# Optimization experiments

Hardware: AMD Instinct MI355X
Metric: run time of the kernel (lower is better)

## Reference

```python
import jax, jax.numpy as jnp
import numpy as np

NUM_HEADS = 16

def setup_inputs() -> dict:
    key = jax.random.key(0)
    ks = jax.random.split(key, 5)
    b, n, d = 2, 2048, 1024
    s = 0.02
    return {
        "x": jax.random.normal(ks[0], (b, n, d), jnp.float32),
        "wq": jax.random.normal(ks[1], (d, d), jnp.float32) * s,
        "wk": jax.random.normal(ks[2], (d, d), jnp.float32) * s,
        "wv": jax.random.normal(ks[3], (d, d), jnp.float32) * s,
        "wo": jax.random.normal(ks[4], (d, d), jnp.float32) * s,
        "bo": jnp.zeros((d,), jnp.float32),
    }

def reference(x, wq, wk, wv, wo, bo):
    b, n, c = x.shape
    h = NUM_HEADS
    hd = c // h
    scale = hd ** -0.5
    # qkv projections (qkv_bias=False); torch Linear computes x @ W.T
    def split_heads(t):
        return t.reshape(b, n, h, hd).transpose(0, 2, 1, 3)  # b h n d
    q = split_heads(x @ wq.T)
    k = split_heads(x @ wk.T)
    v = split_heads(x @ wv.T)
    dots = jnp.einsum('bhid,bhjd->bhij', q, k) * scale
    attn = jax.nn.softmax(dots, axis=-1)  # attn_drop=0 -> identity
    out = jnp.einsum('bhij,bhjd->bhid', attn, v)
    out = out.transpose(0, 2, 1, 3).reshape(b, n, c)
    out = out @ wo.T + bo  # proj_drop=0 -> identity
    return out
```

## Files before the change

kernel.cpp:

```cpp
#include <hip/hip_runtime.h>
#include <hip/hip_bf16.h>

typedef float f32x4 __attribute__((ext_vector_type(4)));
typedef short short8 __attribute__((ext_vector_type(8)));
typedef short short4v __attribute__((ext_vector_type(4)));

#define MFMA(a, b, c) __builtin_amdgcn_mfma_f32_16x16x32_bf16((a), (b), (c), 0, 0, 0)

#if __has_builtin(__builtin_amdgcn_exp2f)
#define EXP2(x) __builtin_amdgcn_exp2f(x)
#else
#define EXP2(x) exp2f(x)
#endif

#define B_  2
#define N_  2048
#define C_  1024
#define H_  16
#define HD_ 64
#define M_  (B_ * N_)

#define QSCALE 0.18033688011112042f

typedef const __attribute__((address_space(1))) void* gp_t;
typedef __attribute__((address_space(3))) void* sp_t;
#define GLL16(g, s) __builtin_amdgcn_global_load_lds((gp_t)(const void*)(g), (sp_t)(void*)(s), 16, 0, 0)

__device__ __forceinline__ short f2bf(float f) {
    union { float fv; unsigned u; } v; v.fv = f;
    unsigned r = v.u + 0x7fffu + ((v.u >> 16) & 1u);
    return (short)(r >> 16);
}
__device__ __forceinline__ unsigned pack_rne(float a, float b) {
    return (unsigned)(unsigned short)f2bf(a) | ((unsigned)(unsigned short)f2bf(b) << 16);
}

__global__ __launch_bounds__(256) void convert_kernel(
    const float* __restrict__ x,  const float* __restrict__ wq,
    const float* __restrict__ wk, const float* __restrict__ wv,
    const float* __restrict__ wo, short* __restrict__ dst)
{
    size_t e = ((size_t)blockIdx.x * 256 + threadIdx.x) * 8;
    const float* src; size_t off;
    if (e < 4194304)      { src = x;  off = e; }
    else if (e < 5242880) { src = wq; off = e - 4194304; }
    else if (e < 6291456) { src = wk; off = e - 5242880; }
    else if (e < 7340032) { src = wv; off = e - 6291456; }
    else                  { src = wo; off = e - 7340032; }
    float4 a = *(const float4*)(src + off);
    float4 b = *(const float4*)(src + off + 4);
    short8 s;
    s[0] = f2bf(a.x); s[1] = f2bf(a.y); s[2] = f2bf(a.z); s[3] = f2bf(a.w);
    s[4] = f2bf(b.x); s[5] = f2bf(b.y); s[6] = f2bf(b.z); s[7] = f2bf(b.w);
    *(short8*)(dst + e) = s;
}

__global__ __launch_bounds__(256) void qkv_gemm(
    const short* __restrict__ xb, const short* __restrict__ Wb,
    short* __restrict__ Qb, short* __restrict__ Kb, short* __restrict__ Vt)
{
    const int m0 = blockIdx.x * 128;
    const int n0 = blockIdx.y * 128;
    __shared__ short As[128 * 64];
    __shared__ short Bs[128 * 64];
    const int tid  = threadIdx.x;
    const int wave = tid >> 6, lane = tid & 63;
    const int quad = lane >> 4, l16 = lane & 15;
    const int wr = (wave >> 1) * 64, wc = (wave & 1) * 64;
    const int sw = l16 & 7;

    const int rS = tid >> 3;
    const int cS = (tid & 7) ^ (rS & 7);
    const short* A_src = xb + (size_t)(m0 + rS) * C_ + cS * 8;
    const short* B_src = Wb + (size_t)(n0 + rS) * C_ + cS * 8;

    f32x4 acc[4][4] = {};

    for (int kk = 0; kk < C_; kk += 64) {
        __syncthreads();
        #pragma unroll
        for (int it = 0; it < 4; ++it) {
            GLL16(A_src + (size_t)(it * 32) * C_ + kk, &As[it * 2048 + tid * 8]);
            GLL16(B_src + (size_t)(it * 32) * C_ + kk, &Bs[it * 2048 + tid * 8]);
        }
        __syncthreads();
        short8 af[4][2], bf[4][2];
        #pragma unroll
        for (int mi = 0; mi < 4; ++mi) {
            int row = (wr + mi * 16 + l16) * 64;
            af[mi][0] = *(const short8*)&As[row + ((quad    ) ^ sw) * 8];
            af[mi][1] = *(const short8*)&As[row + ((quad + 4) ^ sw) * 8];
        }
        #pragma unroll
        for (int ni = 0; ni < 4; ++ni) {
            int row = (wc + ni * 16 + l16) * 64;
            bf[ni][0] = *(const short8*)&Bs[row + ((quad    ) ^ sw) * 8];
            bf[ni][1] = *(const short8*)&Bs[row + ((quad + 4) ^ sw) * 8];
        }
        #pragma unroll
        for (int k2 = 0; k2 < 2; ++k2)
        #pragma unroll
        for (int mi = 0; mi < 4; ++mi)
        #pragma unroll
        for (int ni = 0; ni < 4; ++ni)
            acc[mi][ni] = MFMA(af[mi][k2], bf[ni][k2], acc[mi][ni]);
    }

    const int which = n0 >> 10;
    const int nb = n0 & 1023;
    #pragma unroll
    for (int mi = 0; mi < 4; ++mi)
    #pragma unroll
    for (int ni = 0; ni < 4; ++ni)
    #pragma unroll
    for (int r = 0; r < 4; ++r) {
        int m  = m0 + wr + mi * 16 + quad * 4 + r;
        int cc = nb + wc + ni * 16 + l16;
        float av = acc[mi][ni][r];
        if (which == 0) av *= QSCALE;
        short bv = f2bf(av);
        int bb = m >> 11, ns = m & (N_ - 1);
        int h = cc >> 6, d = cc & 63;
        size_t bh = (size_t)(bb * H_ + h);
        if (which == 0)      Qb[(bh * N_ + ns) * HD_ + d] = bv;
        else if (which == 1) Kb[(bh * N_ + ns) * HD_ + d] = bv;
        else                 Vt[(bh * HD_ + d) * N_ + ns] = bv;
    }
}

__global__ __launch_bounds__(256, 4) void attn_split(
    const short* __restrict__ Qb, const short* __restrict__ Kb,
    const short* __restrict__ Vt, float* __restrict__ Opart,
    float* __restrict__ lpart)
{
    const int bid = blockIdx.x;
    const int swz = (bid & 7) * 128 + (bid >> 3);
    const int bh = swz >> 5;
    const int i0 = ((swz >> 1) & 15) * 128;
    const int sp = swz & 1;
    __shared__ short Ks[2][64 * 64];
    __shared__ short Vs[2][64 * 64];
    const int tid  = threadIdx.x;
    const int wave = tid >> 6, lane = tid & 63;
    const int quad = lane >> 4, l16 = lane & 15;
    const int sw = l16 & 7;

    const short* Qg = Qb + ((size_t)bh * N_ + i0) * HD_;
    const short* Kg = Kb + (size_t)bh * N_ * HD_;
    const short* Vg = Vt + (size_t)bh * HD_ * N_;

    const int row0 = tid >> 3,  c0 = (tid & 7) ^ (row0 & 7);
    const int row1 = row0 + 32, c1 = (tid & 7) ^ (row1 & 7);
    const short* KgA0 = Kg + (sp * 1024 + row0) * HD_ + c0 * 8;
    const short* KgA1 = Kg + (sp * 1024 + row1) * HD_ + c1 * 8;
    const short* VgA0 = Vg + (size_t)row0 * N_ + sp * 1024 + c0 * 8;
    const short* VgA1 = Vg + (size_t)row1 * N_ + sp * 1024 + c1 * 8;

    short8 qf[2][2];
    #pragma unroll
    for (int s = 0; s < 2; ++s) {
        const short* qrow = Qg + (wave * 32 + s * 16 + l16) * HD_;
        qf[s][0] = *(const short8*)(qrow + quad * 8);
        qf[s][1] = *(const short8*)(qrow + quad * 8 + 32);
    }

    GLL16(KgA0, &Ks[0][tid * 8]);
    GLL16(KgA1, &Ks[0][(tid + 256) * 8]);
    GLL16(VgA0, &Vs[0][tid * 8]);
    GLL16(VgA1, &Vs[0][(tid + 256) * 8]);
    __syncthreads();

    f32x4 o[2][4] = {};
    float lrow[2] = {0.f, 0.f};

    for (int jt = 0; jt < 16; ++jt) {
        const int cur = jt & 1;
        if (jt + 1 < 16) {
            int j1 = (jt + 1) * 64;
            GLL16(KgA0 + (size_t)j1 * HD_, &Ks[cur ^ 1][tid * 8]);
            GLL16(KgA1 + (size_t)j1 * HD_, &Ks[cur ^ 1][(tid + 256) * 8]);
            GLL16(VgA0 + j1, &Vs[cur ^ 1][tid * 8]);
            GLL16(VgA1 + j1, &Vs[cur ^ 1][(tid + 256) * 8]);
        }
        const short* Kc = Ks[cur];
        const short* Vc = Vs[cur];

        #pragma unroll
        for (int half = 0; half < 2; ++half) {
            unsigned pq[2][4];
            #pragma unroll
            for (int nio = 0; nio < 2; ++nio) {
                int ni = half * 2 + nio;
                int krow = (ni * 16 + l16) * 64;
                short8 kf0 = *(const short8*)&Kc[krow + ((quad ^ sw) * 8)];
                short8 kf1 = *(const short8*)&Kc[krow + (((quad + 4) ^ sw) * 8)];
                #pragma unroll
                for (int s = 0; s < 2; ++s) {
                    f32x4 st = {0.f, 0.f, 0.f, 0.f};
                    __builtin_amdgcn_s_setprio(1);
                    st = MFMA(kf0, qf[s][0], st);
                    st = MFMA(kf1, qf[s][1], st);
                    __builtin_amdgcn_s_setprio(0);
                    union { float f; unsigned u; } e0, e1, e2, e3;
                    e0.f = EXP2(st[0]); e1.f = EXP2(st[1]);
                    e2.f = EXP2(st[2]); e3.f = EXP2(st[3]);
                    lrow[s] += (e0.f + e1.f) + (e2.f + e3.f);
                    pq[s][nio * 2]     = __builtin_amdgcn_perm(e1.u, e0.u, 0x07060302u);
                    pq[s][nio * 2 + 1] = __builtin_amdgcn_perm(e3.u, e2.u, 0x07060302u);
                }
            }
            #pragma unroll
            for (int di = 0; di < 4; ++di) {
                int vrow = (di * 16 + l16) * 64;
                int ch1 = (half * 4 +     (quad >> 1)) ^ sw;
                int ch2 = (half * 4 + 2 + (quad >> 1)) ^ sw;
                union { struct { short4v lo, hi; } p; short8 v; } va;
                va.p.lo = *(const short4v*)&Vc[vrow + ch1 * 8 + (quad & 1) * 4];
                va.p.hi = *(const short4v*)&Vc[vrow + ch2 * 8 + (quad & 1) * 4];
                __builtin_amdgcn_s_setprio(1);
                #pragma unroll
                for (int s = 0; s < 2; ++s) {
                    union { unsigned u[4]; short8 v; } pb;
                    pb.u[0] = pq[s][0]; pb.u[1] = pq[s][1];
                    pb.u[2] = pq[s][2]; pb.u[3] = pq[s][3];
                    o[s][di] = MFMA(va.v, pb.v, o[s][di]);
                }
                __builtin_amdgcn_s_setprio(0);
            }
        }
        __syncthreads();
    }

    #pragma unroll
    for (int s = 0; s < 2; ++s) {
        float l = lrow[s];
        l += __shfl_xor(l, 16, 64);
        l += __shfl_xor(l, 32, 64);
        int ig = i0 + wave * 32 + s * 16 + l16;
        float* obase = Opart + ((size_t)(sp * 32 + bh) * N_ + ig) * HD_;
        #pragma unroll
        for (int di = 0; di < 4; ++di)
            *(f32x4*)(obase + di * 16 + quad * 4) = o[s][di];
        if (quad == 0) lpart[sp * 65536 + bh * N_ + ig] = l;
    }
}

__global__ __launch_bounds__(256) void merge_kernel(
    const float* __restrict__ Opart, const float* __restrict__ lpart,
    short* __restrict__ Ob)
{
    int e8 = (blockIdx.x * 256 + threadIdx.x) * 8;
    int bh = e8 >> 17;
    int rem = e8 & 131071;
    int ig = rem >> 6, d = rem & 63;
    f32x4 a0 = *(const f32x4*)(Opart + e8);
    f32x4 a1 = *(const f32x4*)(Opart + e8 + 4);
    f32x4 b0 = *(const f32x4*)(Opart + 4194304 + e8);
    f32x4 b1 = *(const f32x4*)(Opart + 4194304 + e8 + 4);
    float inv = 1.f / (lpart[bh * N_ + ig] + lpart[65536 + bh * N_ + ig]);
    short8 s;
    s[0] = f2bf((a0[0] + b0[0]) * inv); s[1] = f2bf((a0[1] + b0[1]) * inv);
    s[2] = f2bf((a0[2] + b0[2]) * inv); s[3] = f2bf((a0[3] + b0[3]) * inv);
    s[4] = f2bf((a1[0] + b1[0]) * inv); s[5] = f2bf((a1[1] + b1[1]) * inv);
    s[6] = f2bf((a1[2] + b1[2]) * inv); s[7] = f2bf((a1[3] + b1[3]) * inv);
    int b = bh >> 4, h = bh & (H_ - 1);
    *(short8*)&Ob[((size_t)(b * N_ + ig)) * C_ + h * HD_ + d] = s;
}

__global__ __launch_bounds__(256) void proj_gemm(
    const short* __restrict__ Ob, const short* __restrict__ wob,
    const float* __restrict__ bo, float* __restrict__ out)
{
    const int m0 = blockIdx.x * 64;
    const int n0 = blockIdx.y * 128;
    __shared__ short As[64 * 64];
    __shared__ short Bs[128 * 64];
    const int tid  = threadIdx.x;
    const int wave = tid >> 6, lane = tid & 63;
    const int quad = lane >> 4, l16 = lane & 15;
    const int wr = (wave >> 1) * 32, wc = (wave & 1) * 64;
    const int sw = l16 & 7;

    const int rS = tid >> 3;
    const int cS = (tid & 7) ^ (rS & 7);
    const short* A_src = Ob  + (size_t)(m0 + rS) * C_ + cS * 8;
    const short* B_src = wob + (size_t)(n0 + rS) * C_ + cS * 8;

    f32x4 acc[2][4] = {};

    for (int kk = 0; kk < C_; kk += 64) {
        __syncthreads();
        GLL16(A_src + kk, &As[tid * 8]);
        GLL16(A_src + (size_t)32 * C_ + kk, &As[(tid + 256) * 8]);
        #pragma unroll
        for (int it = 0; it < 4; ++it)
            GLL16(B_src + (size_t)(it * 32) * C_ + kk, &Bs[it * 2048 + tid * 8]);
        __syncthreads();
        short8 af[2][2], bf[4][2];
        #pragma unroll
        for (int mi = 0; mi < 2; ++mi) {
            int row = (wr + mi * 16 + l16) * 64;
            af[mi][0] = *(const short8*)&As[row + ((quad    ) ^ sw) * 8];
            af[mi][1] = *(const short8*)&As[row + ((quad + 4) ^ sw) * 8];
        }
        #pragma unroll
        for (int ni = 0; ni < 4; ++ni) {
            int row = (wc + ni * 16 + l16) * 64;
            bf[ni][0] = *(const short8*)&Bs[row + ((quad    ) ^ sw) * 8];
            bf[ni][1] = *(const short8*)&Bs[row + ((quad + 4) ^ sw) * 8];
        }
        #pragma unroll
        for (int k2 = 0; k2 < 2; ++k2)
        #pragma unroll
        for (int mi = 0; mi < 2; ++mi)
        #pragma unroll
        for (int ni = 0; ni < 4; ++ni)
            acc[mi][ni] = MFMA(af[mi][k2], bf[ni][k2], acc[mi][ni]);
    }

    #pragma unroll
    for (int mi = 0; mi < 2; ++mi)
    #pragma unroll
    for (int ni = 0; ni < 4; ++ni)
    #pragma unroll
    for (int r = 0; r < 4; ++r) {
        int m = m0 + wr + mi * 16 + quad * 4 + r;
        int c = n0 + wc + ni * 16 + l16;
        out[(size_t)m * C_ + c] = acc[mi][ni][r] + bo[c];
    }
}

extern "C" void kernel_launch(void* const* d_in, const int* in_sizes, int n_in,
                              void* d_out, int out_size, void* d_ws, size_t ws_size,
                              hipStream_t stream) {
    const float* x  = (const float*)d_in[0];
    const float* wq = (const float*)d_in[1];
    const float* wk = (const float*)d_in[2];
    const float* wv = (const float*)d_in[3];
    const float* wo = (const float*)d_in[4];
    const float* bo = (const float*)d_in[5];
    float* out = (float*)d_out;

    short* xb  = (short*)d_ws;
    short* Wb  = xb  + 4194304;
    short* wob = Wb  + 3145728;
    short* Qb  = wob + 1048576;
    short* Kb  = Qb  + 4194304;
    short* Vt  = Kb  + 4194304;
    short* Obuf= Vt  + 4194304;
    float* Opart = (float*)(Obuf + 4194304);
    float* lpart = Opart + 2 * 4194304;

    dim3 blk(256);
    convert_kernel<<<4096, blk, 0, stream>>>(x, wq, wk, wv, wo, xb);
    qkv_gemm<<<dim3(M_ / 128, 3072 / 128), blk, 0, stream>>>(xb, Wb, Qb, Kb, Vt);
    attn_split<<<1024, blk, 0, stream>>>(Qb, Kb, Vt, Opart, lpart);
    merge_kernel<<<2048, blk, 0, stream>>>(Opart, lpart, Obuf);
    proj_gemm<<<dim3(M_ / 64, C_ / 128), blk, 0, stream>>>(Obuf, wob, bo, out);
}
```

Baseline: 190.7 us.

## Double-buffer QKV GEMM shared-memory tiles to overlap loads with MFMA

Splits the QKV GEMM's LDS tiles into two ping-pong buffers so the global-to-LDS load of the next K slice is issued before the MFMAs on the current slice. This drops one barrier per iteration. It also raises wave priority around the MFMA block and asks for two blocks per CU in the launch bounds. The cost is double the shared memory (64 KB per block), which can limit occupancy, plus more register pressure.

```diff
diff --git a/kernel.cpp b/kernel.cpp
--- a/kernel.cpp
+++ b/kernel.cpp
@@ -55,14 +55,14 @@
     *(short8*)(dst + e) = s;
 }
 
-__global__ __launch_bounds__(256) void qkv_gemm(
+__global__ __launch_bounds__(256, 2) void qkv_gemm(
     const short* __restrict__ xb, const short* __restrict__ Wb,
     short* __restrict__ Qb, short* __restrict__ Kb, short* __restrict__ Vt)
 {
     const int m0 = blockIdx.x * 128;
     const int n0 = blockIdx.y * 128;
-    __shared__ short As[128 * 64];
-    __shared__ short Bs[128 * 64];
+    __shared__ short As0[128 * 64], Bs0[128 * 64];
+    __shared__ short As1[128 * 64], Bs1[128 * 64];
     const int tid  = threadIdx.x;
     const int wave = tid >> 6, lane = tid & 63;
     const int quad = lane >> 4, l16 = lane & 15;
@@ -74,37 +74,52 @@
     const short* A_src = xb + (size_t)(m0 + rS) * C_ + cS * 8;
     const short* B_src = Wb + (size_t)(n0 + rS) * C_ + cS * 8;
 
+#define QKV_STAGE(AS, BS, kk) do { \
+    _Pragma("unroll") \
+    for (int it = 0; it < 4; ++it) { \
+        GLL16(A_src + (size_t)(it * 32) * C_ + (kk), &AS[it * 2048 + tid * 8]); \
+        GLL16(B_src + (size_t)(it * 32) * C_ + (kk), &BS[it * 2048 + tid * 8]); \
+    } } while (0)
+
+#define QKV_COMPUTE(AS, BS) do { \
+    short8 af[4][2], bf[4][2]; \
+    _Pragma("unroll") \
+    for (int mi = 0; mi < 4; ++mi) { \
+        int row = (wr + mi * 16 + l16) * 64; \
+        af[mi][0] = *(const short8*)&AS[row + ((quad    ) ^ sw) * 8]; \
+        af[mi][1] = *(const short8*)&AS[row + ((quad + 4) ^ sw) * 8]; \
+    } \
+    _Pragma("unroll") \
+    for (int ni = 0; ni < 4; ++ni) { \
+        int row = (wc + ni * 16 + l16) * 64; \
+        bf[ni][0] = *(const short8*)&BS[row + ((quad    ) ^ sw) * 8]; \
+        bf[ni][1] = *(const short8*)&BS[row + ((quad + 4) ^ sw) * 8]; \
+    } \
+    __builtin_amdgcn_s_setprio(1); \
+    _Pragma("unroll") \
+    for (int k2 = 0; k2 < 2; ++k2) \
+    _Pragma("unroll") \
+    for (int mi = 0; mi < 4; ++mi) \
+    _Pragma("unroll") \
+    for (int ni = 0; ni < 4; ++ni) \
+        acc[mi][ni] = MFMA(af[mi][k2], bf[ni][k2], acc[mi][ni]); \
+    __builtin_amdgcn_s_setprio(0); } while (0)
+
     f32x4 acc[4][4] = {};
 
-    for (int kk = 0; kk < C_; kk += 64) {
-        __syncthreads();
-        #pragma unroll
-        for (int it = 0; it < 4; ++it) {
-            GLL16(A_src + (size_t)(it * 32) * C_ + kk, &As[it * 2048 + tid * 8]);
-            GLL16(B_src + (size_t)(it * 32) * C_ + kk, &Bs[it * 2048 + tid * 8]);
-        }
-        __syncthreads();
-        short8 af[4][2], bf[4][2];
-        #pragma unroll
-        for (int mi = 0; mi < 4; ++mi) {
-            int row = (wr + mi * 16 + l16) * 64;
-            af[mi][0] = *(const short8*)&As[row + ((quad    ) ^ sw) * 8];
-            af[mi][1] = *(const short8*)&As[row + ((quad + 4) ^ sw) * 8];
-        }
-        #pragma unroll
-        for (int ni = 0; ni < 4; ++ni) {
-            int row = (wc + ni * 16 + l16) * 64;
-            bf[ni][0] = *(const short8*)&Bs[row + ((quad    ) ^ sw) * 8];
-            bf[ni][1] = *(const short8*)&Bs[row + ((quad + 4) ^ sw) * 8];
-        }
-        #pragma unroll
-        for (int k2 = 0; k2 < 2; ++k2)
-        #pragma unroll
-        for (int mi = 0; mi < 4; ++mi)
-        #pragma unroll
-        for (int ni = 0; ni < 4; ++ni)
-            acc[mi][ni] = MFMA(af[mi][k2], bf[ni][k2], acc[mi][ni]);
-    }
+    QKV_STAGE(As0, Bs0, 0);
+    __syncthreads();
+    for (int t2 = 0; t2 < 8; ++t2) {
+        const int kk1 = t2 * 128 + 64;
+        QKV_STAGE(As1, Bs1, kk1);
+        QKV_COMPUTE(As0, Bs0);
+        __syncthreads();
+        if (t2 < 7) QKV_STAGE(As0, Bs0, kk1 + 64);
+        QKV_COMPUTE(As1, Bs1);
+        __syncthreads();
+    }
+#undef QKV_STAGE
+#undef QKV_COMPUTE
 
     const int which = n0 >> 10;
     const int nb = n0 & 1023;
```

After: 186.9 us. 1.02x faster.
